# Optimization experiments

Hardware: AMD Instinct MI355X
Metric: run time of the kernel (lower is better)

The kernel has to match this reference:

```python
import jax, jax.numpy as jnp
import numpy as np

B, E, C = 128, 16, 128   # batch, n experts (program tokens), module_dim
H = W = 64               # input image size
PROJ, FC, NANS = 512, 1024, 2


def conv2d(x, w, b, padding=1):
    # x: [N,C,H,W], w: [O,I,kh,kw]
    y = jax.lax.conv_general_dilated(
        x, w, (1, 1), [(padding, padding), (padding, padding)],
        dimension_numbers=('NCHW', 'OIHW', 'NCHW'))
    return y + b[None, :, None, None]


def maxpool2(x):
    return jax.lax.reduce_window(x, -jnp.inf, jax.lax.max, (1, 1, 2, 2), (1, 1, 2, 2), 'VALID')


def setup_inputs() -> dict:
    key = jax.random.key(0)
    ks = jax.random.split(key, 12)
    def init(k, shape, fan_in):
        return jax.random.normal(k, shape, jnp.float32) * np.float32(1.0 / np.sqrt(fan_in))
    inp = {}
    inp['image'] = jax.random.normal(ks[0], (B, 3, H, W), jnp.float32)
    inp['question'] = jax.random.randint(ks[1], (B, 8), 0, E)
    # stem: conv3x3 3->C, relu, maxpool2, conv3x3 C->C, relu, maxpool2
    inp['stem_w1'] = init(ks[2], (C, 3, 3, 3), 3 * 9)
    inp['stem_b1'] = jnp.zeros((C,), jnp.float32)
    inp['stem_w2'] = init(ks[3], (C, C, 3, 3), C * 9)
    inp['stem_b2'] = jnp.zeros((C,), jnp.float32)
    # E expert residual blocks, each: conv3x3 C->C, relu, conv3x3 C->C, +res, relu
    inp['exp_w1'] = init(ks[4], (E, C, C, 3, 3), C * 9)
    inp['exp_b1'] = jnp.zeros((E, C), jnp.float32)
    inp['exp_w2'] = init(ks[5], (E, C, C, 3, 3), C * 9)
    inp['exp_b2'] = jnp.zeros((E, C), jnp.float32)
    # classifier: 1x1 conv C->PROJ, relu, maxpool2, flatten, fc->FC, relu, fc->NANS
    inp['proj_w'] = init(ks[6], (PROJ, C, 1, 1), C)
    inp['proj_b'] = jnp.zeros((PROJ,), jnp.float32)
    inp['fc1_w'] = init(ks[7], (FC, PROJ * 8 * 8), PROJ * 8 * 8)
    inp['fc1_b'] = jnp.zeros((FC,), jnp.float32)
    inp['fc2_w'] = init(ks[8], (NANS, FC), FC)
    inp['fc2_b'] = jnp.zeros((NANS,), jnp.float32)
    return inp


def reference(image, question, stem_w1, stem_b1, stem_w2, stem_b2,
              exp_w1, exp_b1, exp_w2, exp_b2,
              proj_w, proj_b, fc1_w, fc1_b, fc2_w, fc2_b):
    # stem -> [B, C, 16, 16]
    h = maxpool2(jax.nn.relu(conv2d(image, stem_w1, stem_b1)))
    h = maxpool2(jax.nn.relu(conv2d(h, stem_w2, stem_b2)))

    def block(x, w1, b1, w2, b2):
        # per-sample residual block with per-sample expert weights; x: [C,h,w]
        x4 = x[None]
        out = jax.nn.relu(conv2d(x4, w1, b1))
        out = conv2d(out, w2, b2)
        return jax.nn.relu(x4 + out)[0]

    # dispatch order matches [color_lhs, lhs, color_rhs, rhs, rel] = cols 3,4,6,7,5
    for col in (3, 4, 6, 7, 5):
        idx = question[:, col]
        h = jax.vmap(block)(h, exp_w1[idx], exp_b1[idx], exp_w2[idx], exp_b2[idx])

    # classifier
    p = maxpool2(jax.nn.relu(conv2d(h, proj_w, proj_b, padding=0)))  # [B,PROJ,8,8]
    f = p.reshape(p.shape[0], -1)
    f = jax.nn.relu(f @ fc1_w.T + fc1_b)
    return f @ fc2_w.T + fc2_b
```

## Files before the change

kernel.cpp:

```cpp
#include <hip/hip_runtime.h>
#include <hip/hip_bf16.h>
#include <cstdint>
#include <cstddef>


typedef __bf16 bf16_t;
typedef __attribute__((ext_vector_type(4))) bf16_t bf16x4;
typedef __attribute__((ext_vector_type(8))) bf16_t bf16x8;
typedef __attribute__((ext_vector_type(16))) float f32x16;
typedef __attribute__((ext_vector_type(4))) float f32x4;

__global__ __launch_bounds__(256) void wconv_frag_k(
    const float* __restrict__ in, bf16_t* __restrict__ out)
{
  const int bid = blockIdx.x;
  const int dd  = bid % 9;
  const int r1  = bid / 9;
  const int ich = r1 & 1;
  const int r2  = r1 >> 1;
  const int ocg = r2 & 3;
  const int e   = r2 >> 2;

  const int t = threadIdx.x;
  const int kh = t >> 6, lane = t & 63;
  const int g = lane >> 5, cc = lane & 31;

  const float* ip = in + (size_t)(e * 128 + ocg * 32 + cc) * 1152 + dd;
  const int ic0 = ich * 64 + kh * 16 + g * 8;

  bf16_t* op = out + (size_t)e * 147456
             + ((size_t)(((ocg * 2 + ich) * 9 + dd) * 4) << 9) + t * 8;
  bf16x8 v;
#pragma unroll
  for (int j = 0; j < 8; ++j) v[j] = (bf16_t)ip[(ic0 + j) * 9];
  *(bf16x8*)op = v;
}

__global__ __launch_bounds__(128) void pconv_frag_k(
    const float* __restrict__ in, bf16_t* __restrict__ out)
{
  const int oc = blockIdx.x;
  const int og = oc >> 5, cc = oc & 31;
  const int ic = threadIdx.x;
  const int ich = ic >> 6, icl = ic & 63;
  const int kh = icl >> 4, g = (icl >> 3) & 1, j = icl & 7;
  const int off = ((((og * 2 + ich) * 4 + kh) << 9)) + ((g << 5) + cc) * 8 + j;
  out[off] = (bf16_t)in[(size_t)oc * 128 + ic];
}

__global__ __launch_bounds__(256) void stem1_nhwc_k(
    const float* __restrict__ img, const float* __restrict__ w1,
    const float* __restrict__ b1, bf16_t* __restrict__ out)
{
  const int bid = blockIdx.x;
  const int b = bid >> 4, t = bid & 15;
  const int ty0p = (t >> 2) * 8, tx0p = (t & 3) * 8;
  const int tid = threadIdx.x, lane = tid & 63;
  const int wvbase = __builtin_amdgcn_readfirstlane(tid >> 6) * 32;

  __shared__ float sImg[3][18][19];
  __shared__ char  sOut[16384];

  for (int s = tid; s < 972; s += 256) {
    const int ic = s / 324, r2 = s - ic * 324;
    const int rr = r2 / 18, cc = r2 - rr * 18;
    const int gy = 2 * ty0p - 1 + rr, gx = 2 * tx0p - 1 + cc;
    float v = 0.f;
    if (gy >= 0 && gy < 64 && gx >= 0 && gx < 64)
      v = img[(((size_t)b * 3 + ic) * 64 + gy) * 64 + gx];
    sImg[ic][rr][cc] = v;
  }
  __syncthreads();

  const int ppy = lane >> 3, ppx = lane & 7;
  float patch[3][4][4];
#pragma unroll
  for (int ic = 0; ic < 3; ++ic)
#pragma unroll
    for (int r = 0; r < 4; ++r)
#pragma unroll
      for (int c = 0; c < 4; ++c)
        patch[ic][r][c] = sImg[ic][2 * ppy + r][2 * ppx + c];

  const int swz = (lane & 15) << 3;
  char* orow = sOut + lane * 256;
#pragma unroll 2
  for (int o4 = 0; o4 < 32; o4 += 4) {
    bf16x4 qv;
#pragma unroll
    for (int j = 0; j < 4; ++j) {
      const int oc = wvbase + o4 + j;
      const float* wp = w1 + oc * 27;
      float a[2][2];
#pragma unroll
      for (int i = 0; i < 2; ++i)
#pragma unroll
        for (int jj = 0; jj < 2; ++jj) a[i][jj] = b1[oc];
#pragma unroll
      for (int ic = 0; ic < 3; ++ic)
#pragma unroll
        for (int dy = 0; dy < 3; ++dy)
#pragma unroll
          for (int dx = 0; dx < 3; ++dx) {
            const float wv = wp[ic * 9 + dy * 3 + dx];
#pragma unroll
            for (int i = 0; i < 2; ++i)
#pragma unroll
              for (int jj = 0; jj < 2; ++jj)
                a[i][jj] = fmaf(patch[ic][i + dy][jj + dx], wv, a[i][jj]);
          }
      const float mx = fmaxf(fmaxf(a[0][0], a[0][1]), fmaxf(a[1][0], a[1][1]));
      qv[j] = (bf16_t)fmaxf(mx, 0.f);
    }
    *(bf16x4*)(orow + (((wvbase + o4) * 2) ^ swz)) = qv;
  }
  __syncthreads();

#pragma unroll
  for (int it = 0; it < 4; ++it) {
    const int idx = it * 256 + tid;
    const int px = idx >> 4, ch8 = idx & 15;
    const int sw = (px & 15) << 3;
    const char* rb = sOut + px * 256;
    bf16x4 lo = *(const bf16x4*)(rb + ((ch8 * 16) ^ sw));
    bf16x4 hi = *(const bf16x4*)(rb + ((ch8 * 16 + 8) ^ sw));
    bf16x8 v;
#pragma unroll
    for (int j = 0; j < 4; ++j) { v[j] = lo[j]; v[4 + j] = hi[j]; }
    const int gpy = ty0p + (px >> 3), gpx = tx0p + (px & 7);
    *(bf16x8*)(out + ((size_t)(b * 1024 + gpy * 32 + gpx)) * 128 + ch8 * 8) = v;
  }
}

__global__ __launch_bounds__(256) void conv_stem2_k(
    const bf16_t* __restrict__ act, const bf16_t* __restrict__ wF,
    const float* __restrict__ bias, bf16_t* __restrict__ out)
{
  const int b = blockIdx.x >> 2, ph = blockIdx.x & 3;
  const int y0 = ph * 8;
  const int tid = threadIdx.x, lane = tid & 63, wv = tid >> 6;
  const int g = lane >> 5, cc = lane & 31;
  const int wq_oc = wv & 1, wq_px = wv >> 1;

  __shared__ bf16_t simg[10 * 34 * 64];

  f32x16 acc[2][4];
#pragma unroll
  for (int i = 0; i < 2; ++i)
#pragma unroll
    for (int j = 0; j < 4; ++j)
#pragma unroll
      for (int r = 0; r < 16; ++r) acc[i][j][r] = 0.f;

  int sl[4];
#pragma unroll
  for (int nf = 0; nf < 4; ++nf) sl[nf] = (wq_px * 4 + nf) * 34 + cc;

  const bf16_t* wfb = wF + (((size_t)(wq_oc * 2) * 2) * 9 * 4 << 9) + lane * 8;

  for (int ich = 0; ich < 2; ++ich) {
    __syncthreads();
    for (int p = tid; p < 340; p += 256) {
      const int yy = p / 34, xx = p - yy * 34;
      const int gy = y0 + yy - 1, gx = xx - 1;
      const bool inb = (gy >= 0 && gy < 32 && gx >= 0 && gx < 32);
      const bf16_t* src = act + ((size_t)(b * 1024 + gy * 32 + gx)) * 128 + ich * 64;
#pragma unroll
      for (int j = 0; j < 8; ++j) {
        bf16x8 v = {};
        if (inb) v = *(const bf16x8*)(src + j * 8);
        const int waddr = (p * 128 + j * 16) ^ ((p & 7) << 4);
        *(bf16x8*)((char*)simg + waddr) = v;
      }
    }
    __syncthreads();

    for (int dydx = 0; dydx < 9; ++dydx) {
      const int dy = dydx / 3, dx = dydx - dy * 3;
      const int sb = dy * 34 + dx;
      const bf16_t* wf = wfb + (((ich * 9 + dydx) * 4) << 9);
#pragma unroll
      for (int kh = 0; kh < 4; ++kh) {
        const bf16x8 a0 = *(const bf16x8*)(wf + (kh << 9));
        const bf16x8 a1 = *(const bf16x8*)(wf + 36864 + (kh << 9));
#pragma unroll
        for (int nf = 0; nf < 4; ++nf) {
          const int s = sl[nf] + sb;
          const int raddr = (s * 128 + (kh * 2 + g) * 16) ^ ((s & 7) << 4);
          const bf16x8 bbv = *(const bf16x8*)((const char*)simg + raddr);
          acc[0][nf] = __builtin_amdgcn_mfma_f32_32x32x16_bf16(a0, bbv, acc[0][nf], 0, 0, 0);
          acc[1][nf] = __builtin_amdgcn_mfma_f32_32x32x16_bf16(a1, bbv, acc[1][nf], 0, 0, 0);
        }
      }
    }
  }

#pragma unroll
  for (int mf = 0; mf < 2; ++mf) {
#pragma unroll
    for (int q = 0; q < 2; ++q) {
      const int py = (y0 + wq_px * 4 + 2 * q) >> 1;
      const int pxp = cc >> 1;
      bf16_t* op = out + ((size_t)(b * 256 + py * 16 + pxp)) * 128;
#pragma unroll
      for (int rq = 0; rq < 4; ++rq) {
        const int oc4 = wq_oc * 64 + mf * 32 + rq * 8 + g * 4;
        const f32x4 bi = *(const f32x4*)(bias + oc4);
        bf16x4 qv;
#pragma unroll
        for (int j = 0; j < 4; ++j) {
          const int r = rq * 4 + j;
          float v = fmaxf(acc[mf][2 * q][r], acc[mf][2 * q + 1][r]);
          v = fmaxf(v, __shfl_xor(v, 1));
          qv[j] = (bf16_t)fmaxf(v + bi[j], 0.f);
        }
        if ((cc & 1) == 0) *(bf16x4*)(op + oc4) = qv;
      }
    }
  }
}

template<int RES>
__global__ __launch_bounds__(256) void conv_exp_k(
    const bf16_t* __restrict__ act, const bf16_t* __restrict__ wF,
    const float* __restrict__ bias, const int* __restrict__ question, int col,
    const bf16_t* __restrict__ res, bf16_t* __restrict__ out)
{
  const int b = blockIdx.x >> 2, ph = blockIdx.x & 3;
  const int y0 = ph * 4;
  const int e = question[b * 8 + col];
  const int tid = threadIdx.x, lane = tid & 63, wv = tid >> 6;
  const int g = lane >> 5, cc = lane & 31;
  const int wq_oc = wv & 1, wq_px = wv >> 1;

  __shared__ bf16_t simg[216 * 64];

  f32x16 acc[2];
#pragma unroll
  for (int i = 0; i < 2; ++i)
#pragma unroll
    for (int r = 0; r < 16; ++r) acc[i][r] = 0.f;

  const int px = wq_px * 32 + cc;
  const int sl = (px >> 4) * 18 + (px & 15);

  const bf16_t* wfb = wF + (size_t)e * 147456
                    + (((size_t)(wq_oc * 2) * 2) * 9 * 4 << 9) + lane * 8;

  for (int p = tid; p < 216; p += 256) {
    const int ich = p / 108, r2 = p - ich * 108;
    const int yy = r2 / 18, xx = r2 - yy * 18;
    const int gy = y0 + yy - 1, gx = xx - 1;
    const bool inb = (gy >= 0 && gy < 16 && gx >= 0 && gx < 16);
    const bf16_t* src = act + ((size_t)(b * 256 + gy * 16 + gx)) * 128 + ich * 64;
#pragma unroll
    for (int j = 0; j < 8; ++j) {
      bf16x8 v = {};
      if (inb) v = *(const bf16x8*)(src + j * 8);
      const int waddr = (p * 128 + j * 16) ^ ((p & 7) << 4);
      *(bf16x8*)((char*)simg + waddr) = v;
    }
  }
  __syncthreads();

#pragma unroll
  for (int ich = 0; ich < 2; ++ich) {
    for (int dydx = 0; dydx < 9; ++dydx) {
      const int dy = dydx / 3, dx = dydx - dy * 3;
      const int sbase = ich * 108 + sl + dy * 18 + dx;
      const bf16_t* wf = wfb + (((ich * 9 + dydx) * 4) << 9);
#pragma unroll
      for (int kh = 0; kh < 4; ++kh) {
        const bf16x8 a0 = *(const bf16x8*)(wf + (kh << 9));
        const bf16x8 a1 = *(const bf16x8*)(wf + 36864 + (kh << 9));
        const int raddr = (sbase * 128 + (kh * 2 + g) * 16) ^ ((sbase & 7) << 4);
        const bf16x8 bbv = *(const bf16x8*)((const char*)simg + raddr);
        acc[0] = __builtin_amdgcn_mfma_f32_32x32x16_bf16(a0, bbv, acc[0], 0, 0, 0);
        acc[1] = __builtin_amdgcn_mfma_f32_32x32x16_bf16(a1, bbv, acc[1], 0, 0, 0);
      }
    }
  }

  const float* bb = bias + e * 128;
  const size_t pixbase = ((size_t)(b * 256 + (y0 + (px >> 4)) * 16 + (px & 15))) * 128;
  bf16_t* op = out + pixbase;
#pragma unroll
  for (int mf = 0; mf < 2; ++mf) {
#pragma unroll
    for (int rq = 0; rq < 4; ++rq) {
      const int oc4 = wq_oc * 64 + mf * 32 + rq * 8 + g * 4;
      const f32x4 bi = *(const f32x4*)(bb + oc4);
      bf16x4 qv;
      bf16x4 rv = {};
      if (RES) rv = *(const bf16x4*)(res + pixbase + oc4);
#pragma unroll
      for (int j = 0; j < 4; ++j) {
        float v = acc[mf][rq * 4 + j] + bi[j];
        if (RES) v += (float)rv[j];
        qv[j] = (bf16_t)fmaxf(v, 0.f);
      }
      *(bf16x4*)(op + oc4) = qv;
    }
  }
}

__global__ __launch_bounds__(256) void proj_mfma_k(
    const bf16_t* __restrict__ h, const bf16_t* __restrict__ pwF,
    const float* __restrict__ pb, bf16_t* __restrict__ f)
{
  const int b = blockIdx.x >> 2, ocg = blockIdx.x & 3;
  const int tid = threadIdx.x, lane = tid & 63, wv = tid >> 6;
  const int g = lane >> 5, cc = lane & 31;
  const int wq_oc = wv & 1, wq_px = wv >> 1;

  __shared__ bf16_t simg[256 * 64];

  f32x16 acc[2][4];
#pragma unroll
  for (int i = 0; i < 2; ++i)
#pragma unroll
    for (int j = 0; j < 4; ++j)
#pragma unroll
      for (int r = 0; r < 16; ++r) acc[i][j][r] = 0.f;

  const int px0 = wq_px * 128 + cc;
  const int og0 = ocg * 4 + wq_oc * 2;
  const bf16_t* pfb = pwF + (((size_t)og0 * 2 * 4) << 9) + lane * 8;

  for (int ich = 0; ich < 2; ++ich) {
    __syncthreads();
    {
      const int p = tid;
      const bf16_t* src = h + ((size_t)(b * 256 + p)) * 128 + ich * 64;
#pragma unroll
      for (int j = 0; j < 8; ++j) {
        bf16x8 v = *(const bf16x8*)(src + j * 8);
        const int waddr = (p * 128 + j * 16) ^ ((p & 7) << 4);
        *(bf16x8*)((char*)simg + waddr) = v;
      }
    }
    __syncthreads();

#pragma unroll
    for (int kh = 0; kh < 4; ++kh) {
      const bf16x8 a0 = *(const bf16x8*)(pfb + ((ich * 4 + kh) << 9));
      const bf16x8 a1 = *(const bf16x8*)(pfb + 4096 + ((ich * 4 + kh) << 9));
#pragma unroll
      for (int nf = 0; nf < 4; ++nf) {
        const int s = px0 + nf * 32;
        const int raddr = (s * 128 + (kh * 2 + g) * 16) ^ ((s & 7) << 4);
        const bf16x8 bb = *(const bf16x8*)((const char*)simg + raddr);
        acc[0][nf] = __builtin_amdgcn_mfma_f32_32x32x16_bf16(a0, bb, acc[0][nf], 0, 0, 0);
        acc[1][nf] = __builtin_amdgcn_mfma_f32_32x32x16_bf16(a1, bb, acc[1][nf], 0, 0, 0);
      }
    }
  }

#pragma unroll
  for (int mf = 0; mf < 2; ++mf) {
#pragma unroll
    for (int nf = 0; nf < 4; ++nf) {
      const int px = px0 + nf * 32;
      const int x = px & 15;
      const int py = wq_px * 4 + nf;
      const int pxp = x >> 1;
#pragma unroll
      for (int r = 0; r < 16; ++r) {
        float v = acc[mf][nf][r];
        v = fmaxf(v, __shfl_xor(v, 1));
        v = fmaxf(v, __shfl_xor(v, 16));
        const int oc = ocg * 128 + wq_oc * 64 + mf * 32 + (r & 3) + 8 * (r >> 2) + 4 * g;
        v = fmaxf(v + pb[oc], 0.f);
        if ((cc & 17) == 0)
          f[((size_t)(b * 512 + oc)) * 64 + py * 8 + pxp] = (bf16_t)v;
      }
    }
  }
}

__global__ __launch_bounds__(256) void fc1_mfma_k(
    const bf16_t* __restrict__ A, const float* __restrict__ W,
    float* __restrict__ part)
{
  const int nt = blockIdx.x;
  const int ks = blockIdx.y;
  const int n0 = nt * 64;
  const int k0 = ks * 1024;
  const int tid = threadIdx.x, lane = tid & 63, wv = tid >> 6;
  const int g = lane >> 5, cc = lane & 31;
  const int mh = wv & 1, nh = wv >> 1;

  __shared__ char sA[16384];
  __shared__ char sB[8192];

  f32x16 acc0, acc1;
#pragma unroll
  for (int r = 0; r < 16; ++r) { acc0[r] = 0.f; acc1[r] = 0.f; }

  for (int t = 0; t < 16; ++t) {
    __syncthreads();
#pragma unroll
    for (int i = 0; i < 4; ++i) {
      const int c = tid + i * 256;
      const int row = c >> 3, ko = c & 7;
      bf16x8 v = *(const bf16x8*)(A + (size_t)row * 32768 + k0 + t * 64 + ko * 8);
      const int wa = (row * 128 + ko * 16) ^ ((row & 7) << 4);
      *(bf16x8*)(sA + wa) = v;
    }
#pragma unroll
    for (int i = 0; i < 2; ++i) {
      const int c = tid + i * 256;
      const int row = c >> 3, ko = c & 7;
      const float* src = W + (size_t)(n0 + row) * 32768 + k0 + t * 64 + ko * 8;
      f32x4 u0 = *(const f32x4*)src;
      f32x4 u1 = *(const f32x4*)(src + 4);
      bf16x8 v;
#pragma unroll
      for (int j = 0; j < 4; ++j) { v[j] = (bf16_t)u0[j]; v[4 + j] = (bf16_t)u1[j]; }
      const int wa = (row * 128 + ko * 16) ^ ((row & 7) << 4);
      *(bf16x8*)(sB + wa) = v;
    }
    __syncthreads();
#pragma unroll
    for (int kss = 0; kss < 4; ++kss) {
      const int kb = kss * 32 + g * 16;
      const int rA0 = mh * 64 + cc, rA1 = rA0 + 32;
      const bf16x8 a0 = *(const bf16x8*)(sA + ((rA0 * 128 + kb) ^ ((rA0 & 7) << 4)));
      const bf16x8 a1 = *(const bf16x8*)(sA + ((rA1 * 128 + kb) ^ ((rA1 & 7) << 4)));
      const int rB = nh * 32 + cc;
      const bf16x8 bb = *(const bf16x8*)(sB + ((rB * 128 + kb) ^ ((rB & 7) << 4)));
      acc0 = __builtin_amdgcn_mfma_f32_32x32x16_bf16(a0, bb, acc0, 0, 0, 0);
      acc1 = __builtin_amdgcn_mfma_f32_32x32x16_bf16(a1, bb, acc1, 0, 0, 0);
    }
  }

  float* pp = part + ((size_t)ks * 128) * 1024 + n0 + nh * 32 + cc;
#pragma unroll
  for (int r = 0; r < 16; ++r) {
    const int m0 = mh * 64 + (r & 3) + 8 * (r >> 2) + 4 * g;
    pp[(size_t)m0 * 1024] = acc0[r];
    pp[(size_t)(m0 + 32) * 1024] = acc1[r];
  }
}

__global__ __launch_bounds__(256) void fc1_red_k(
    const float* __restrict__ part, const float* __restrict__ bias, float* __restrict__ fo)
{
  const int i = blockIdx.x * 256 + threadIdx.x;
  const int m = i >> 10, j = i & 1023;
  float s = bias[j];
#pragma unroll
  for (int ks = 0; ks < 32; ++ks) s += part[((size_t)ks * 128 + m) * 1024 + j];
  fo[i] = fmaxf(s, 0.f);
}

__global__ __launch_bounds__(256) void fc2_k(
    const float* __restrict__ fo, const float* __restrict__ w2,
    const float* __restrict__ b2, float* __restrict__ out)
{
  const int m = blockIdx.x;
  const int tid = threadIdx.x;
  float a0 = 0.f, a1 = 0.f;
  for (int k = tid; k < 1024; k += 256) {
    const float fv = fo[(size_t)m * 1024 + k];
    a0 = fmaf(fv, w2[k], a0);
    a1 = fmaf(fv, w2[1024 + k], a1);
  }
#pragma unroll
  for (int o = 32; o > 0; o >>= 1) {
    a0 += __shfl_down(a0, o);
    a1 += __shfl_down(a1, o);
  }
  __shared__ float r0[4], r1[4];
  const int wid = tid >> 6;
  if ((tid & 63) == 0) { r0[wid] = a0; r1[wid] = a1; }
  __syncthreads();
  if (tid == 0) {
    out[(size_t)m * 2 + 0] = r0[0] + r0[1] + r0[2] + r0[3] + b2[0];
    out[(size_t)m * 2 + 1] = r1[0] + r1[1] + r1[2] + r1[3] + b2[1];
  }
}

extern "C" void kernel_launch(void* const* d_in, const int* in_sizes, int n_in,
                              void* d_out, int out_size, void* d_ws, size_t ws_size,
                              hipStream_t stream)
{
  const float* image    = (const float*)d_in[0];
  const int*   question = (const int*)  d_in[1];
  const float* stem_w1  = (const float*)d_in[2];
  const float* stem_b1  = (const float*)d_in[3];
  const float* stem_w2  = (const float*)d_in[4];
  const float* stem_b2  = (const float*)d_in[5];
  const float* exp_w1   = (const float*)d_in[6];
  const float* exp_b1   = (const float*)d_in[7];
  const float* exp_w2   = (const float*)d_in[8];
  const float* exp_b2   = (const float*)d_in[9];
  const float* proj_w   = (const float*)d_in[10];
  const float* proj_b   = (const float*)d_in[11];
  const float* fc1_w    = (const float*)d_in[12];
  const float* fc1_b    = (const float*)d_in[13];
  const float* fc2_w    = (const float*)d_in[14];
  const float* fc2_b    = (const float*)d_in[15];
  float* out = (float*)d_out;

  char* base = (char*)d_ws;
  bf16_t* actA   = (bf16_t*)(base + 33554432);
  bf16_t* actH   = (bf16_t*)(base + 67108864);
  bf16_t* actT   = (bf16_t*)(base + 75497472);
  bf16_t* wT1    = (bf16_t*)(base + 83886080);
  bf16_t* wT2    = (bf16_t*)(base + 88604672);
  bf16_t* wTs2   = (bf16_t*)(base + 93323264);
  bf16_t* pwT    = (bf16_t*)(base + 93618176);
  bf16_t* fbf  = (bf16_t*)base;
  float*  part = (float*)(base + 8388608);
  float*  f1o  = (float*)(base + 25165824);

  wconv_frag_k<<<1152, 256, 0, stream>>>(exp_w1, wT1);
  wconv_frag_k<<<1152, 256, 0, stream>>>(exp_w2, wT2);
  wconv_frag_k<<<72, 256, 0, stream>>>(stem_w2, wTs2);
  pconv_frag_k<<<512, 128, 0, stream>>>(proj_w, pwT);

  stem1_nhwc_k<<<2048, 256, 0, stream>>>(image, stem_w1, stem_b1, actA);
  conv_stem2_k<<<512, 256, 0, stream>>>(actA, wTs2, stem_b2, actH);

  const int cols[5] = {3, 4, 6, 7, 5};
  for (int i = 0; i < 5; ++i) {
    conv_exp_k<0><<<512, 256, 0, stream>>>(actH, wT1, exp_b1, question, cols[i],
                                           nullptr, actT);
    conv_exp_k<1><<<512, 256, 0, stream>>>(actT, wT2, exp_b2, question, cols[i],
                                           actH, actH);
  }

  proj_mfma_k<<<512, 256, 0, stream>>>(actH, pwT, proj_b, fbf);
  fc1_mfma_k<<<dim3(16, 32), 256, 0, stream>>>(fbf, fc1_w, part);
  fc1_red_k<<<512, 256, 0, stream>>>(part, fc1_b, f1o);
  fc2_k<<<128, 256, 0, stream>>>(f1o, fc2_w, fc2_b, out);
}
```

Baseline: 387.9 us.

## Split expert conv across input-channel halves and retile fc1 with larger N tiles

The expert conv kernel now gives each block two output rows instead of four and doubles the grid. Its four waves split the input-channel dimension in two, and the partial accumulators are reduced through shared memory before the epilogue. This is meant to raise parallelism and occupancy on the dominant conv stage, at the cost of an extra LDS reduction, a barrier, and half the waves idling in the epilogue. Separately, fc1 uses 128-wide N tiles with a 2x2 MFMA tile per wave and twice as many K splits, which doubles the partial-sum buffer that the reduction kernel must read.

```diff
diff --git a/kernel.cpp b/kernel.cpp
--- a/kernel.cpp
+++ b/kernel.cpp
@@ -226,14 +226,15 @@
     const float* __restrict__ bias, const int* __restrict__ question, int col,
     const bf16_t* __restrict__ res, bf16_t* __restrict__ out)
 {
-  const int b = blockIdx.x >> 2, ph = blockIdx.x & 3;
-  const int y0 = ph * 4;
+  const int b = blockIdx.x >> 3, ph = blockIdx.x & 7;
+  const int y0 = ph * 2;
   const int e = question[b * 8 + col];
   const int tid = threadIdx.x, lane = tid & 63, wv = tid >> 6;
   const int g = lane >> 5, cc = lane & 31;
-  const int wq_oc = wv & 1, wq_px = wv >> 1;
-
-  __shared__ bf16_t simg[216 * 64];
+  const int wq_oc = wv & 1, wq_ic = wv >> 1;
+
+  __shared__ bf16_t simg[144 * 64];
+  __shared__ float sRed[4096];
 
   f32x16 acc[2];
 #pragma unroll
@@ -241,14 +242,13 @@
 #pragma unroll
     for (int r = 0; r < 16; ++r) acc[i][r] = 0.f;
 
-  const int px = wq_px * 32 + cc;
-  const int sl = (px >> 4) * 18 + (px & 15);
+  const int xr = cc >> 4, x = cc & 15;
 
   const bf16_t* wfb = wF + (size_t)e * 147456
                     + (((size_t)(wq_oc * 2) * 2) * 9 * 4 << 9) + lane * 8;
 
-  for (int p = tid; p < 216; p += 256) {
-    const int ich = p / 108, r2 = p - ich * 108;
+  for (int p = tid; p < 144; p += 256) {
+    const int ich = p / 72, r2 = p - ich * 72;
     const int yy = r2 / 18, xx = r2 - yy * 18;
     const int gy = y0 + yy - 1, gx = xx - 1;
     const bool inb = (gy >= 0 && gy < 16 && gx >= 0 && gx < 16);
@@ -263,43 +263,57 @@
   }
   __syncthreads();
 
-#pragma unroll
-  for (int ich = 0; ich < 2; ++ich) {
-    for (int dydx = 0; dydx < 9; ++dydx) {
-      const int dy = dydx / 3, dx = dydx - dy * 3;
-      const int sbase = ich * 108 + sl + dy * 18 + dx;
-      const bf16_t* wf = wfb + (((ich * 9 + dydx) * 4) << 9);
-#pragma unroll
-      for (int kh = 0; kh < 4; ++kh) {
-        const bf16x8 a0 = *(const bf16x8*)(wf + (kh << 9));
-        const bf16x8 a1 = *(const bf16x8*)(wf + 36864 + (kh << 9));
-        const int raddr = (sbase * 128 + (kh * 2 + g) * 16) ^ ((sbase & 7) << 4);
-        const bf16x8 bbv = *(const bf16x8*)((const char*)simg + raddr);
-        acc[0] = __builtin_amdgcn_mfma_f32_32x32x16_bf16(a0, bbv, acc[0], 0, 0, 0);
-        acc[1] = __builtin_amdgcn_mfma_f32_32x32x16_bf16(a1, bbv, acc[1], 0, 0, 0);
-      }
-    }
-  }
-
-  const float* bb = bias + e * 128;
-  const size_t pixbase = ((size_t)(b * 256 + (y0 + (px >> 4)) * 16 + (px & 15))) * 128;
-  bf16_t* op = out + pixbase;
-#pragma unroll
-  for (int mf = 0; mf < 2; ++mf) {
-#pragma unroll
-    for (int rq = 0; rq < 4; ++rq) {
-      const int oc4 = wq_oc * 64 + mf * 32 + rq * 8 + g * 4;
-      const f32x4 bi = *(const f32x4*)(bb + oc4);
-      bf16x4 qv;
-      bf16x4 rv = {};
-      if (RES) rv = *(const bf16x4*)(res + pixbase + oc4);
-#pragma unroll
-      for (int j = 0; j < 4; ++j) {
-        float v = acc[mf][rq * 4 + j] + bi[j];
-        if (RES) v += (float)rv[j];
-        qv[j] = (bf16_t)fmaxf(v, 0.f);
-      }
-      *(bf16x4*)(op + oc4) = qv;
+  const int ichS = wq_ic * 72;
+  for (int dydx = 0; dydx < 9; ++dydx) {
+    const int dy = dydx / 3, dx = dydx - dy * 3;
+    const int sbase = ichS + (xr + dy) * 18 + (x + dx);
+    const bf16_t* wf = wfb + (((wq_ic * 9 + dydx) * 4) << 9);
+#pragma unroll
+    for (int kh = 0; kh < 4; ++kh) {
+      const bf16x8 a0 = *(const bf16x8*)(wf + (kh << 9));
+      const bf16x8 a1 = *(const bf16x8*)(wf + 36864 + (kh << 9));
+      const int raddr = (sbase * 128 + (kh * 2 + g) * 16) ^ ((sbase & 7) << 4);
+      const bf16x8 bbv = *(const bf16x8*)((const char*)simg + raddr);
+      acc[0] = __builtin_amdgcn_mfma_f32_32x32x16_bf16(a0, bbv, acc[0], 0, 0, 0);
+      acc[1] = __builtin_amdgcn_mfma_f32_32x32x16_bf16(a1, bbv, acc[1], 0, 0, 0);
+    }
+  }
+
+  if (wq_ic == 1) {
+#pragma unroll
+    for (int mf = 0; mf < 2; ++mf)
+#pragma unroll
+      for (int r = 0; r < 16; ++r)
+        sRed[((wq_oc * 2 + mf) * 16 + r) * 64 + lane] = acc[mf][r];
+  }
+  __syncthreads();
+  if (wq_ic == 0) {
+#pragma unroll
+    for (int mf = 0; mf < 2; ++mf)
+#pragma unroll
+      for (int r = 0; r < 16; ++r)
+        acc[mf][r] += sRed[((wq_oc * 2 + mf) * 16 + r) * 64 + lane];
+
+    const float* bb = bias + e * 128;
+    const size_t pixbase = ((size_t)(b * 256 + (y0 + xr) * 16 + x)) * 128;
+    bf16_t* op = out + pixbase;
+#pragma unroll
+    for (int mf = 0; mf < 2; ++mf) {
+#pragma unroll
+      for (int rq = 0; rq < 4; ++rq) {
+        const int oc4 = wq_oc * 64 + mf * 32 + rq * 8 + g * 4;
+        const f32x4 bi = *(const f32x4*)(bb + oc4);
+        bf16x4 qv;
+        bf16x4 rv = {};
+        if (RES) rv = *(const bf16x4*)(res + pixbase + oc4);
+#pragma unroll
+        for (int j = 0; j < 4; ++j) {
+          float v = acc[mf][rq * 4 + j] + bi[j];
+          if (RES) v += (float)rv[j];
+          qv[j] = (bf16_t)fmaxf(v, 0.f);
+        }
+        *(bf16x4*)(op + oc4) = qv;
+      }
     }
   }
 }
@@ -384,20 +398,24 @@
 {
   const int nt = blockIdx.x;
   const int ks = blockIdx.y;
-  const int n0 = nt * 64;
-  const int k0 = ks * 1024;
+  const int n0 = nt * 128;
+  const int k0 = ks * 512;
   const int tid = threadIdx.x, lane = tid & 63, wv = tid >> 6;
   const int g = lane >> 5, cc = lane & 31;
   const int mh = wv & 1, nh = wv >> 1;
 
   __shared__ char sA[16384];
-  __shared__ char sB[8192];
-
-  f32x16 acc0, acc1;
-#pragma unroll
-  for (int r = 0; r < 16; ++r) { acc0[r] = 0.f; acc1[r] = 0.f; }
-
-  for (int t = 0; t < 16; ++t) {
+  __shared__ char sB[16384];
+
+  f32x16 acc[2][2];
+#pragma unroll
+  for (int im = 0; im < 2; ++im)
+#pragma unroll
+    for (int in = 0; in < 2; ++in)
+#pragma unroll
+      for (int r = 0; r < 16; ++r) acc[im][in][r] = 0.f;
+
+  for (int t = 0; t < 8; ++t) {
     __syncthreads();
 #pragma unroll
     for (int i = 0; i < 4; ++i) {
@@ -408,7 +426,7 @@
       *(bf16x8*)(sA + wa) = v;
     }
 #pragma unroll
-    for (int i = 0; i < 2; ++i) {
+    for (int i = 0; i < 4; ++i) {
       const int c = tid + i * 256;
       const int row = c >> 3, ko = c & 7;
       const float* src = W + (size_t)(n0 + row) * 32768 + k0 + t * 64 + ko * 8;
@@ -425,22 +443,29 @@
     for (int kss = 0; kss < 4; ++kss) {
       const int kb = kss * 32 + g * 16;
       const int rA0 = mh * 64 + cc, rA1 = rA0 + 32;
+      const int rB0 = nh * 64 + cc, rB1 = rB0 + 32;
       const bf16x8 a0 = *(const bf16x8*)(sA + ((rA0 * 128 + kb) ^ ((rA0 & 7) << 4)));
       const bf16x8 a1 = *(const bf16x8*)(sA + ((rA1 * 128 + kb) ^ ((rA1 & 7) << 4)));
-      const int rB = nh * 32 + cc;
-      const bf16x8 bb = *(const bf16x8*)(sB + ((rB * 128 + kb) ^ ((rB & 7) << 4)));
-      acc0 = __builtin_amdgcn_mfma_f32_32x32x16_bf16(a0, bb, acc0, 0, 0, 0);
-      acc1 = __builtin_amdgcn_mfma_f32_32x32x16_bf16(a1, bb, acc1, 0, 0, 0);
-    }
-  }
-
-  float* pp = part + ((size_t)ks * 128) * 1024 + n0 + nh * 32 + cc;
-#pragma unroll
-  for (int r = 0; r < 16; ++r) {
-    const int m0 = mh * 64 + (r & 3) + 8 * (r >> 2) + 4 * g;
-    pp[(size_t)m0 * 1024] = acc0[r];
-    pp[(size_t)(m0 + 32) * 1024] = acc1[r];
-  }
+      const bf16x8 b0 = *(const bf16x8*)(sB + ((rB0 * 128 + kb) ^ ((rB0 & 7) << 4)));
+      const bf16x8 b1 = *(const bf16x8*)(sB + ((rB1 * 128 + kb) ^ ((rB1 & 7) << 4)));
+      acc[0][0] = __builtin_amdgcn_mfma_f32_32x32x16_bf16(a0, b0, acc[0][0], 0, 0, 0);
+      acc[0][1] = __builtin_amdgcn_mfma_f32_32x32x16_bf16(a0, b1, acc[0][1], 0, 0, 0);
+      acc[1][0] = __builtin_amdgcn_mfma_f32_32x32x16_bf16(a1, b0, acc[1][0], 0, 0, 0);
+      acc[1][1] = __builtin_amdgcn_mfma_f32_32x32x16_bf16(a1, b1, acc[1][1], 0, 0, 0);
+    }
+  }
+
+#pragma unroll
+  for (int im = 0; im < 2; ++im)
+#pragma unroll
+    for (int in = 0; in < 2; ++in) {
+      float* pp = part + ((size_t)ks * 128) * 1024 + n0 + nh * 64 + in * 32 + cc;
+#pragma unroll
+      for (int r = 0; r < 16; ++r) {
+        const int m0 = mh * 64 + im * 32 + (r & 3) + 8 * (r >> 2) + 4 * g;
+        pp[(size_t)m0 * 1024] = acc[im][in][r];
+      }
+    }
 }
 
 __global__ __launch_bounds__(256) void fc1_red_k(
@@ -449,8 +474,8 @@
   const int i = blockIdx.x * 256 + threadIdx.x;
   const int m = i >> 10, j = i & 1023;
   float s = bias[j];
-#pragma unroll
-  for (int ks = 0; ks < 32; ++ks) s += part[((size_t)ks * 128 + m) * 1024 + j];
+#pragma unroll 8
+  for (int ks = 0; ks < 64; ++ks) s += part[((size_t)ks * 128 + m) * 1024 + j];
   fo[i] = fmaxf(s, 0.f);
 }
 
@@ -513,7 +538,7 @@
   bf16_t* pwT    = (bf16_t*)(base + 93618176);
   bf16_t* fbf  = (bf16_t*)base;
   float*  part = (float*)(base + 8388608);
-  float*  f1o  = (float*)(base + 25165824);
+  float*  f1o  = (float*)(base + 41943040);
 
   wconv_frag_k<<<1152, 256, 0, stream>>>(exp_w1, wT1);
   wconv_frag_k<<<1152, 256, 0, stream>>>(exp_w2, wT2);
@@ -525,14 +550,14 @@
 
   const int cols[5] = {3, 4, 6, 7, 5};
   for (int i = 0; i < 5; ++i) {
-    conv_exp_k<0><<<512, 256, 0, stream>>>(actH, wT1, exp_b1, question, cols[i],
-                                           nullptr, actT);
-    conv_exp_k<1><<<512, 256, 0, stream>>>(actT, wT2, exp_b2, question, cols[i],
-                                           actH, actH);
+    conv_exp_k<0><<<1024, 256, 0, stream>>>(actH, wT1, exp_b1, question, cols[i],
+                                            nullptr, actT);
+    conv_exp_k<1><<<1024, 256, 0, stream>>>(actT, wT2, exp_b2, question, cols[i],
+                                            actH, actH);
   }
 
   proj_mfma_k<<<512, 256, 0, stream>>>(actH, pwT, proj_b, fbf);
-  fc1_mfma_k<<<dim3(16, 32), 256, 0, stream>>>(fbf, fc1_w, part);
+  fc1_mfma_k<<<dim3(8, 64), 256, 0, stream>>>(fbf, fc1_w, part);
   fc1_red_k<<<512, 256, 0, stream>>>(part, fc1_b, f1o);
   fc2_k<<<128, 256, 0, stream>>>(f1o, fc2_w, fc2_b, out);
 }
```

Result: slower. 478.4 us (+23.3%).

## Retile stem conv2 to two-row blocks with one channel slab per wave

Applied to the files above, without the earlier changes.

The second stem conv now launches 2048 blocks, each covering two output rows (one pooled row) instead of eight. Each wave owns 32 output channels and two pixel rows, so the accumulators shrink from eight tiles to two. Both input-channel halves are staged into shared memory with a single barrier, and the tap loops are fully unrolled, including in the expert conv. The aim is more parallelism and occupancy through lower register and LDS pressure per block, at the cost of re-reading more halo rows and loading the weights more often per output.

```diff
diff --git a/kernel.cpp b/kernel.cpp
--- a/kernel.cpp
+++ b/kernel.cpp
@@ -136,87 +136,73 @@
     const bf16_t* __restrict__ act, const bf16_t* __restrict__ wF,
     const float* __restrict__ bias, bf16_t* __restrict__ out)
 {
-  const int b = blockIdx.x >> 2, ph = blockIdx.x & 3;
-  const int y0 = ph * 8;
+  const int b = blockIdx.x >> 4, ph = blockIdx.x & 15;
+  const int y0 = ph * 2;
   const int tid = threadIdx.x, lane = tid & 63, wv = tid >> 6;
   const int g = lane >> 5, cc = lane & 31;
-  const int wq_oc = wv & 1, wq_px = wv >> 1;
-
-  __shared__ bf16_t simg[10 * 34 * 64];
-
-  f32x16 acc[2][4];
+  const int wq = wv;
+
+  __shared__ bf16_t simg[272 * 64];
+
+  f32x16 acc[2];
 #pragma unroll
   for (int i = 0; i < 2; ++i)
 #pragma unroll
-    for (int j = 0; j < 4; ++j)
-#pragma unroll
-      for (int r = 0; r < 16; ++r) acc[i][j][r] = 0.f;
-
-  int sl[4];
-#pragma unroll
-  for (int nf = 0; nf < 4; ++nf) sl[nf] = (wq_px * 4 + nf) * 34 + cc;
-
-  const bf16_t* wfb = wF + (((size_t)(wq_oc * 2) * 2) * 9 * 4 << 9) + lane * 8;
-
+    for (int r = 0; r < 16; ++r) acc[i][r] = 0.f;
+
+  const bf16_t* wfb = wF + ((size_t)(wq * 2) * 9 * 4 << 9) + lane * 8;
+
+  for (int p = tid; p < 272; p += 256) {
+    const int ich = p / 136, r2 = p - ich * 136;
+    const int yy = r2 / 34, xx = r2 - yy * 34;
+    const int gy = y0 + yy - 1, gx = xx - 1;
+    const bool inb = (gy >= 0 && gy < 32 && gx >= 0 && gx < 32);
+    const bf16_t* src = act + ((size_t)(b * 1024 + gy * 32 + gx)) * 128 + ich * 64;
+#pragma unroll
+    for (int j = 0; j < 8; ++j) {
+      bf16x8 v = {};
+      if (inb) v = *(const bf16x8*)(src + j * 8);
+      const int waddr = (p * 128 + j * 16) ^ ((p & 7) << 4);
+      *(bf16x8*)((char*)simg + waddr) = v;
+    }
+  }
+  __syncthreads();
+
+#pragma unroll
   for (int ich = 0; ich < 2; ++ich) {
-    __syncthreads();
-    for (int p = tid; p < 340; p += 256) {
-      const int yy = p / 34, xx = p - yy * 34;
-      const int gy = y0 + yy - 1, gx = xx - 1;
-      const bool inb = (gy >= 0 && gy < 32 && gx >= 0 && gx < 32);
-      const bf16_t* src = act + ((size_t)(b * 1024 + gy * 32 + gx)) * 128 + ich * 64;
-#pragma unroll
-      for (int j = 0; j < 8; ++j) {
-        bf16x8 v = {};
-        if (inb) v = *(const bf16x8*)(src + j * 8);
-        const int waddr = (p * 128 + j * 16) ^ ((p & 7) << 4);
-        *(bf16x8*)((char*)simg + waddr) = v;
-      }
-    }
-    __syncthreads();
-
+#pragma unroll
     for (int dydx = 0; dydx < 9; ++dydx) {
       const int dy = dydx / 3, dx = dydx - dy * 3;
-      const int sb = dy * 34 + dx;
       const bf16_t* wf = wfb + (((ich * 9 + dydx) * 4) << 9);
 #pragma unroll
       for (int kh = 0; kh < 4; ++kh) {
-        const bf16x8 a0 = *(const bf16x8*)(wf + (kh << 9));
-        const bf16x8 a1 = *(const bf16x8*)(wf + 36864 + (kh << 9));
-#pragma unroll
-        for (int nf = 0; nf < 4; ++nf) {
-          const int s = sl[nf] + sb;
+        const bf16x8 a = *(const bf16x8*)(wf + (kh << 9));
+#pragma unroll
+        for (int r = 0; r < 2; ++r) {
+          const int s = ich * 136 + (r + 1 + dy - 1) * 34 + cc + dx;
           const int raddr = (s * 128 + (kh * 2 + g) * 16) ^ ((s & 7) << 4);
           const bf16x8 bbv = *(const bf16x8*)((const char*)simg + raddr);
-          acc[0][nf] = __builtin_amdgcn_mfma_f32_32x32x16_bf16(a0, bbv, acc[0][nf], 0, 0, 0);
-          acc[1][nf] = __builtin_amdgcn_mfma_f32_32x32x16_bf16(a1, bbv, acc[1][nf], 0, 0, 0);
+          acc[r] = __builtin_amdgcn_mfma_f32_32x32x16_bf16(a, bbv, acc[r], 0, 0, 0);
         }
       }
     }
   }
 
-#pragma unroll
-  for (int mf = 0; mf < 2; ++mf) {
-#pragma unroll
-    for (int q = 0; q < 2; ++q) {
-      const int py = (y0 + wq_px * 4 + 2 * q) >> 1;
-      const int pxp = cc >> 1;
-      bf16_t* op = out + ((size_t)(b * 256 + py * 16 + pxp)) * 128;
-#pragma unroll
-      for (int rq = 0; rq < 4; ++rq) {
-        const int oc4 = wq_oc * 64 + mf * 32 + rq * 8 + g * 4;
-        const f32x4 bi = *(const f32x4*)(bias + oc4);
-        bf16x4 qv;
-#pragma unroll
-        for (int j = 0; j < 4; ++j) {
-          const int r = rq * 4 + j;
-          float v = fmaxf(acc[mf][2 * q][r], acc[mf][2 * q + 1][r]);
-          v = fmaxf(v, __shfl_xor(v, 1));
-          qv[j] = (bf16_t)fmaxf(v + bi[j], 0.f);
-        }
-        if ((cc & 1) == 0) *(bf16x4*)(op + oc4) = qv;
-      }
-    }
+  const int pxp = cc >> 1;
+  bf16_t* op = out + ((size_t)(b * 256 + ph * 16 + pxp)) * 128;
+#pragma unroll
+  for (int rq = 0; rq < 4; ++rq) {
+    const int oc4 = wq * 32 + rq * 8 + g * 4;
+    const f32x4 bi = *(const f32x4*)(bias + oc4);
+    bf16x4 qv;
+#pragma unroll
+    for (int j = 0; j < 4; ++j) {
+      const int r = rq * 4 + j;
+      float v = fmaxf(acc[0][r], acc[1][r]);
+      v = fmaxf(v, __shfl_xor(v, 1));
+      qv[j] = (bf16_t)fmaxf(v + bi[j], 0.f);
+    }
+    if ((cc & 1) == 0) *(bf16x4*)(op + oc4) = qv;
   }
 }
 
@@ -265,6 +251,7 @@
 
 #pragma unroll
   for (int ich = 0; ich < 2; ++ich) {
+#pragma unroll
     for (int dydx = 0; dydx < 9; ++dydx) {
       const int dy = dydx / 3, dx = dydx - dy * 3;
       const int sbase = ich * 108 + sl + dy * 18 + dx;
@@ -521,7 +508,7 @@
   pconv_frag_k<<<512, 128, 0, stream>>>(proj_w, pwT);
 
   stem1_nhwc_k<<<2048, 256, 0, stream>>>(image, stem_w1, stem_b1, actA);
-  conv_stem2_k<<<512, 256, 0, stream>>>(actA, wTs2, stem_b2, actH);
+  conv_stem2_k<<<2048, 256, 0, stream>>>(actA, wTs2, stem_b2, actH);
 
   const int cols[5] = {3, 4, 6, 7, 5};
   for (int i = 0; i < 5; ++i) {
```

New measurement: 380.6 us. About the same (-1.9%).
